# Kernel optimization log

Hardware: AMD Instinct MI355X
Metric: run time of the kernel (lower is better)

Reference implementation:

```python
import jax, jax.numpy as jnp
import numpy as np


def hadamard_matrix(n):
    # Recursive normalized Hadamard matrix of size 2^n (matches the torch code).
    H = np.array([[1.0]])
    for _ in range(n):
        H = np.block([[H, H], [H, -H]]) / np.sqrt(2.0)
    return jnp.asarray(H, dtype=jnp.float32)


def hadamard_conv(x, filt, bias, H):
    # x: (B, Cin, h, w); filt: (F, kh, kw); bias: (F, 1); H: (n, n)
    n = H.shape[0]
    F, kh, kw = filt.shape
    B, C = x.shape[0], x.shape[1]
    # zero-pad filters and data up to (n, n), then 2D Hadamard transform H A H
    kern = jnp.zeros((F, n, n), x.dtype).at[:, :kh, :kw].set(filt)
    kern_t = jnp.matmul(H, jnp.matmul(kern, H))            # (F, n, n)
    data = jnp.zeros((B, C, n, n), x.dtype).at[:, :, : x.shape[2], : x.shape[3]].set(x)
    data_t = jnp.matmul(H, jnp.matmul(data, H))            # (B, C, n, n)
    # Original: expand to (B, C, F, n, n), multiply by kern_t, inverse transform,
    # then sum over C. Since kern_t is independent of C and the transforms are
    # linear, sum over C first -- identical math, no huge intermediate.
    s = data_t.sum(axis=1)                                  # (B, n, n)
    prod = s[:, None, :, :] * kern_t[None, :, :, :]         # (B, F, n, n)
    out = jnp.matmul(H, jnp.matmul(prod, H))                # (B, F, n, n)
    return out + bias[:, 0][None, :, None, None]


def maxpool2(x):
    # 2x2 max pool, stride 2, on (B, C, H, W)
    return jax.lax.reduce_window(x, -jnp.inf, jax.lax.max, (1, 1, 2, 2), (1, 1, 2, 2), 'VALID')


def setup_inputs() -> dict:
    key = jax.random.key(0)
    ks = jax.random.split(key, 9)
    return {
        'x': jax.random.normal(ks[0], (2048, 3, 32, 32), dtype=jnp.float32),
        'filter1': jax.random.normal(ks[1], (32, 3, 3), dtype=jnp.float32),
        'bias1': jax.random.normal(ks[2], (32, 1), dtype=jnp.float32),
        'filter2': jax.random.normal(ks[3], (64, 3, 3), dtype=jnp.float32),
        'bias2': jax.random.normal(ks[4], (64, 1), dtype=jnp.float32),
        'fc1_w': jax.random.normal(ks[5], (512, 4096), dtype=jnp.float32) * 0.02,
        'fc1_b': jax.random.normal(ks[6], (512,), dtype=jnp.float32) * 0.02,
        'fc2_w': jax.random.normal(ks[7], (10, 512), dtype=jnp.float32) * 0.02,
        'fc2_b': jax.random.normal(ks[8], (10,), dtype=jnp.float32) * 0.02,
    }


def reference(x, filter1, bias1, filter2, bias2, fc1_w, fc1_b, fc2_w, fc2_b):
    H1 = hadamard_matrix(5)  # 32x32
    H2 = hadamard_matrix(4)  # 16x16
    out = hadamard_conv(x, filter1, bias1, H1)      # (B, 32, 32, 32)
    out = maxpool2(jax.nn.relu(out))                # (B, 32, 16, 16)
    out = hadamard_conv(out, filter2, bias2, H2)    # (B, 64, 16, 16)
    out = maxpool2(jax.nn.relu(out))                # (B, 64, 8, 8)
    out = out.reshape(-1, 4096)
    out = jax.nn.relu(out @ fc1_w.T + fc1_b)        # (B, 512)
    out = out @ fc2_w.T + fc2_b                     # (B, 10)
    return jax.nn.softmax(out, axis=1)
```

## Files before the change

### kernel.cpp

```cpp
#include <hip/hip_runtime.h>

#define DEVI __device__ __forceinline__

typedef __attribute__((ext_vector_type(8))) short short8x;
typedef __attribute__((ext_vector_type(4))) float float4x;

DEVI float shx(float v, int m) { return __shfl_xor(v, m, 64); }

DEVI unsigned bf16r(float v) {
  unsigned u = __float_as_uint(v);
  return (u + 0x7FFF + ((u >> 16) & 1)) >> 16;
}
DEVI void split2(float a, float b, unsigned& h, unsigned& l) {
  unsigned ra = bf16r(a), rb = bf16r(b);
  float fa = __uint_as_float(ra << 16), fb = __uint_as_float(rb << 16);
  unsigned la = bf16r(a - fa), lb = bf16r(b - fb);
  h = ra | (rb << 16);
  l = la | (lb << 16);
}

DEVI void gload16(const void* g, void* l) {
  __builtin_amdgcn_global_load_lds(
      (const __attribute__((address_space(1))) void*)g,
      (__attribute__((address_space(3))) void*)l, 16, 0, 0);
}

template <int MASK>
DEVI float lanex(float x) {
  if constexpr (MASK == 1)
    return __int_as_float(__builtin_amdgcn_update_dpp(
        0, __float_as_int(x), 0xB1, 0xF, 0xF, true));
  else if constexpr (MASK == 2)
    return __int_as_float(__builtin_amdgcn_update_dpp(
        0, __float_as_int(x), 0x4E, 0xF, 0xF, true));
  else
    return __int_as_float(__builtin_amdgcn_ds_swizzle(
        __float_as_int(x), (MASK << 10) | 0x1F));
}

__global__ __launch_bounds__(256) void k_conv(
    const float* __restrict__ x, const float* __restrict__ filt1,
    const float* __restrict__ bias1, const float* __restrict__ filt2,
    const float* __restrict__ bias2, unsigned short* __restrict__ Ah,
    unsigned short* __restrict__ Al) {
  __shared__ float sP[4 * 320];
  const int b = blockIdx.x;
  const int tid = threadIdx.x;
  const int wv = tid >> 6, t = tid & 63;

  float s0[16];
  {
    const float* xb = x + (size_t)b * 3072 + (t >> 1) * 32 + (t & 1) * 16;
#pragma unroll
    for (int q = 0; q < 4; ++q) {
      float4 a0 = *(const float4*)(xb + 4 * q);
      float4 a1 = *(const float4*)(xb + 1024 + 4 * q);
      float4 a2 = *(const float4*)(xb + 2048 + 4 * q);
      s0[4 * q + 0] = a0.x + a1.x + a2.x;
      s0[4 * q + 1] = a0.y + a1.y + a2.y;
      s0[4 * q + 2] = a0.z + a1.z + a2.z;
      s0[4 * q + 3] = a0.w + a1.w + a2.w;
    }
  }
  float s1[16], s2[16];
#pragma unroll
  for (int k = 0; k < 16; ++k) s1[k] = lanex<2>(s0[k]);
#pragma unroll
  for (int k = 0; k < 16; ++k) s2[k] = lanex<4>(s0[k]);

  float acc[8];
#pragma unroll
  for (int j = 0; j < 8; ++j) acc[j] = 0.0f;

  for (int i = 0; i < 8; ++i) {
    const int f = __builtin_amdgcn_readfirstlane(wv * 8 + i);
    const float* fp = filt1 + f * 9;
    float w[9];
#pragma unroll
    for (int k = 0; k < 9; ++k) w[k] = fp[k] * (1.0f / 32.0f);
    const float bb = bias1[f];
    float u[16];
#pragma unroll
    for (int jj = 0; jj < 16; ++jj) {
      const int j1 = jj ^ 1, j2 = jj ^ 2;
      float v = fmaf(w[0], s0[jj], bb);
      v = fmaf(w[1], s0[j1], v);
      v = fmaf(w[2], s0[j2], v);
      v = fmaf(w[3], s1[jj], v);
      v = fmaf(w[4], s1[j1], v);
      v = fmaf(w[5], s1[j2], v);
      v = fmaf(w[6], s2[jj], v);
      v = fmaf(w[7], s2[j1], v);
      v = fmaf(w[8], s2[j2], v);
      u[jj] = fmaxf(v, 0.0f);
    }
#pragma unroll
    for (int k = 0; k < 16; ++k) u[k] = fmaxf(u[k], lanex<2>(u[k]));
#pragma unroll
    for (int j = 0; j < 8; ++j) acc[j] += fmaxf(u[2 * j], u[2 * j + 1]);
  }

  if (!(t & 2)) {
    const int pb = wv * 320 + (t >> 2) * 20 + (t & 1) * 8;
    *(float4*)&sP[pb] = make_float4(acc[0], acc[1], acc[2], acc[3]);
    *(float4*)&sP[pb + 4] = make_float4(acc[4], acc[5], acc[6], acc[7]);
  }
  __syncthreads();

  const int f2s = t >> 4, rr = t & 15;
  float r0[16];
#pragma unroll
  for (int q = 0; q < 4; ++q) {
    float4 s = make_float4(0.f, 0.f, 0.f, 0.f);
#pragma unroll
    for (int w2 = 0; w2 < 4; ++w2) {
      const float4 v = *(const float4*)&sP[w2 * 320 + rr * 20 + 4 * q];
      s.x += v.x; s.y += v.y; s.z += v.z; s.w += v.w;
    }
    r0[4 * q + 0] = s.x;
    r0[4 * q + 1] = s.y;
    r0[4 * q + 2] = s.z;
    r0[4 * q + 3] = s.w;
  }
  float r1[16], r2[16];
#pragma unroll
  for (int k = 0; k < 16; ++k) r1[k] = lanex<1>(r0[k]);
#pragma unroll
  for (int k = 0; k < 16; ++k) r2[k] = lanex<2>(r0[k]);

#pragma unroll
  for (int it = 0; it < 4; ++it) {
    const int g = wv * 16 + it * 4 + f2s;
    const float* gp = filt2 + g * 9;
    float w[9];
#pragma unroll
    for (int k = 0; k < 9; ++k) w[k] = gp[k] * (1.0f / 16.0f);
    const float bb = bias2[g];
    float u[16];
#pragma unroll
    for (int jj = 0; jj < 16; ++jj) {
      const int j1 = jj ^ 1, j2 = jj ^ 2;
      float v = fmaf(w[0], r0[jj], bb);
      v = fmaf(w[1], r0[j1], v);
      v = fmaf(w[2], r0[j2], v);
      v = fmaf(w[3], r1[jj], v);
      v = fmaf(w[4], r1[j1], v);
      v = fmaf(w[5], r1[j2], v);
      v = fmaf(w[6], r2[jj], v);
      v = fmaf(w[7], r2[j1], v);
      v = fmaf(w[8], r2[j2], v);
      u[jj] = fmaxf(v, 0.0f);
    }
#pragma unroll
    for (int k = 0; k < 16; ++k) u[k] = fmaxf(u[k], lanex<1>(u[k]));
    float p[8];
#pragma unroll
    for (int j = 0; j < 8; ++j) p[j] = fmaxf(u[2 * j], u[2 * j + 1]);
    if (!(t & 1)) {
      unsigned hh[4], ll[4];
#pragma unroll
      for (int j = 0; j < 4; ++j) split2(p[2 * j], p[2 * j + 1], hh[j], ll[j]);
      const size_t off = (size_t)b * 4096 + g * 64 + (rr >> 1) * 8;
      *(uint4*)(Ah + off) = make_uint4(hh[0], hh[1], hh[2], hh[3]);
      *(uint4*)(Al + off) = make_uint4(ll[0], ll[1], ll[2], ll[3]);
    }
  }
}

__global__ __launch_bounds__(256) void k_wsplit(
    const float* __restrict__ W, unsigned short* __restrict__ Wh,
    unsigned short* __restrict__ Wl) {
  const int i = (blockIdx.x * 256 + threadIdx.x) * 4;
  float4 v = *(const float4*)(W + i);
  unsigned h0, l0, h1, l1;
  split2(v.x, v.y, h0, l0);
  split2(v.z, v.w, h1, l1);
  *(uint2*)(Wh + i) = make_uint2(h0, h1);
  *(uint2*)(Wl + i) = make_uint2(l0, l1);
}

__global__ __launch_bounds__(256) void k_fc1(
    const unsigned short* __restrict__ Ah, const unsigned short* __restrict__ Al,
    const unsigned short* __restrict__ Wh, const unsigned short* __restrict__ Wl,
    float* __restrict__ P, int M) {
  __shared__ __align__(16) unsigned char lds[49152];
  const int bid = blockIdx.x;
  const int low3 = bid & 7, rest = bid >> 3;
  const int nt = rest & 7;
  const int c = ((rest >> 3) << 3) | low3;
  const int mt = c >> 2, kidx = c & 3;
  const int m0 = mt * 128, n0 = nt * 64, k0 = kidx * 1024;

  const int tid = threadIdx.x;
  const int wv = tid >> 6, lane = tid & 63;
  const int wm = (wv >> 1) * 64, wn = (wv & 1) * 32;
  const int lm = lane & 15, lq = lane >> 4;
  const int lr = lane >> 3, lc = lane & 7;

  float4x acc[4][2];
#pragma unroll
  for (int i = 0; i < 4; ++i)
#pragma unroll
    for (int j = 0; j < 2; ++j) acc[i][j] = (float4x){0.f, 0.f, 0.f, 0.f};

  for (int kk = 0; kk < 1024; kk += 64) {
    const int kcol = k0 + kk;
#pragma unroll
    for (int it = 0; it < 4; ++it) {
      const int rbase = wv * 32 + it * 8;
      const int r = rbase + lr;
      const size_t go = (size_t)(m0 + r) * 4096 + kcol + (lc ^ (r & 7)) * 8;
      gload16(Ah + go, lds + rbase * 128);
      gload16(Al + go, lds + 16384 + rbase * 128);
    }
#pragma unroll
    for (int it = 0; it < 2; ++it) {
      const int rbase = wv * 16 + it * 8;
      const int r = rbase + lr;
      const size_t go = (size_t)(n0 + r) * 4096 + kcol + (lc ^ (r & 7)) * 8;
      gload16(Wh + go, lds + 32768 + rbase * 128);
      gload16(Wl + go, lds + 40960 + rbase * 128);
    }
    __syncthreads();

    const uint4* l4 = (const uint4*)lds;
#pragma unroll
    for (int ks = 0; ks < 2; ++ks) {
      const int ch = ks * 4 + lq;
      short8x a_h[4], a_l[4], b_h[2], b_l[2];
#pragma unroll
      for (int fm = 0; fm < 4; ++fm) {
        const int r = wm + fm * 16 + lm;
        const int s = r * 8 + (ch ^ (r & 7));
        a_h[fm] = *(const short8x*)&l4[s];
        a_l[fm] = *(const short8x*)&l4[1024 + s];
      }
#pragma unroll
      for (int fn = 0; fn < 2; ++fn) {
        const int r = wn + fn * 16 + lm;
        const int s = r * 8 + (ch ^ (r & 7));
        b_h[fn] = *(const short8x*)&l4[2048 + s];
        b_l[fn] = *(const short8x*)&l4[2560 + s];
      }
#pragma unroll
      for (int fm = 0; fm < 4; ++fm)
#pragma unroll
        for (int fn = 0; fn < 2; ++fn) {
          acc[fm][fn] = __builtin_amdgcn_mfma_f32_16x16x32_bf16(
              a_h[fm], b_h[fn], acc[fm][fn], 0, 0, 0);
          acc[fm][fn] = __builtin_amdgcn_mfma_f32_16x16x32_bf16(
              a_h[fm], b_l[fn], acc[fm][fn], 0, 0, 0);
          acc[fm][fn] = __builtin_amdgcn_mfma_f32_16x16x32_bf16(
              a_l[fm], b_h[fn], acc[fm][fn], 0, 0, 0);
        }
    }
    __syncthreads();
  }

  float* Pp = P + (size_t)kidx * ((size_t)M * 512);
#pragma unroll
  for (int fm = 0; fm < 4; ++fm)
#pragma unroll
    for (int fn = 0; fn < 2; ++fn)
#pragma unroll
      for (int i = 0; i < 4; ++i) {
        const int r = m0 + wm + fm * 16 + lq * 4 + i;
        const int cc = n0 + wn + fn * 16 + lm;
        Pp[(size_t)r * 512 + cc] = acc[fm][fn][i];
      }
}

__global__ __launch_bounds__(256) void k_fc1red4(
    const float* __restrict__ P, const float* __restrict__ bias,
    float* __restrict__ O, int total) {
  const int idx = (blockIdx.x * 256 + threadIdx.x) * 4;
  const float4 p0 = *(const float4*)(P + idx);
  const float4 p1 = *(const float4*)(P + (size_t)total + idx);
  const float4 p2 = *(const float4*)(P + (size_t)2 * total + idx);
  const float4 p3 = *(const float4*)(P + (size_t)3 * total + idx);
  const float4 bv = *(const float4*)(bias + (idx & 511));
  float4 o;
  o.x = fmaxf(p0.x + p1.x + p2.x + p3.x + bv.x, 0.0f);
  o.y = fmaxf(p0.y + p1.y + p2.y + p3.y + bv.y, 0.0f);
  o.z = fmaxf(p0.z + p1.z + p2.z + p3.z + bv.z, 0.0f);
  o.w = fmaxf(p0.w + p1.w + p2.w + p3.w + bv.w, 0.0f);
  *(float4*)(O + idx) = o;
}

__global__ __launch_bounds__(256) void k_fc2(
    const float* __restrict__ X, const float* __restrict__ W,
    const float* __restrict__ bias, float* __restrict__ out) {
  const int wv = threadIdx.x >> 6, t = threadIdx.x & 63;
  const int b = blockIdx.x * 4 + wv;
  const float* xr = X + (size_t)b * 512 + t * 8;
  const float4 x0 = *(const float4*)xr;
  const float4 x1 = *(const float4*)(xr + 4);
  float z[10];
#pragma unroll
  for (int o = 0; o < 10; ++o) {
    const float* wr = W + o * 512 + t * 8;
    const float4 w0 = *(const float4*)wr;
    const float4 w1 = *(const float4*)(wr + 4);
    float s = x0.x * w0.x;
    s = fmaf(x0.y, w0.y, s);
    s = fmaf(x0.z, w0.z, s);
    s = fmaf(x0.w, w0.w, s);
    s = fmaf(x1.x, w1.x, s);
    s = fmaf(x1.y, w1.y, s);
    s = fmaf(x1.z, w1.z, s);
    s = fmaf(x1.w, w1.w, s);
    z[o] = s;
  }
#pragma unroll
  for (int m = 1; m < 64; m <<= 1) {
#pragma unroll
    for (int o = 0; o < 10; ++o) z[o] += shx(z[o], m);
  }
#pragma unroll
  for (int o = 0; o < 10; ++o) z[o] += bias[o];
  float mx = z[0];
#pragma unroll
  for (int o = 1; o < 10; ++o) mx = fmaxf(mx, z[o]);
  float e[10];
  float ssum = 0.0f;
#pragma unroll
  for (int o = 0; o < 10; ++o) {
    e[o] = expf(z[o] - mx);
    ssum += e[o];
  }
  const float inv = 1.0f / ssum;
  if (t == 0) {
    float* dst = out + (size_t)b * 10;
#pragma unroll
    for (int o = 0; o < 10; ++o) dst[o] = e[o] * inv;
  }
}

extern "C" void kernel_launch(void* const* d_in, const int* in_sizes, int n_in,
                              void* d_out, int out_size, void* d_ws,
                              size_t ws_size, hipStream_t stream) {
  const float* x = (const float*)d_in[0];
  const float* f1 = (const float*)d_in[1];
  const float* b1 = (const float*)d_in[2];
  const float* f2 = (const float*)d_in[3];
  const float* b2 = (const float*)d_in[4];
  const float* fc1w = (const float*)d_in[5];
  const float* fc1b = (const float*)d_in[6];
  const float* fc2w = (const float*)d_in[7];
  const float* fc2b = (const float*)d_in[8];
  float* out = (float*)d_out;
  const int B = in_sizes[0] / 3072;

  char* w = (char*)d_ws;
  unsigned short* Ah = (unsigned short*)w;
  unsigned short* Al = (unsigned short*)(w + (size_t)B * 8192);
  unsigned short* Wh = (unsigned short*)(w + (size_t)2 * B * 8192);
  unsigned short* Wl = (unsigned short*)(w + (size_t)2 * B * 8192 + 4194304);
  float* P = (float*)(w + (size_t)2 * B * 8192 + 8388608);
  float* fc1o =
      (float*)(w + (size_t)2 * B * 8192 + 8388608 + (size_t)4 * B * 2048);

  hipLaunchKernelGGL(k_wsplit, dim3(2048), dim3(256), 0, stream, fc1w, Wh, Wl);
  hipLaunchKernelGGL(k_conv, dim3(B), dim3(256), 0, stream, x, f1, b1, f2, b2,
                     Ah, Al);
  hipLaunchKernelGGL(k_fc1, dim3((B / 128) * 32), dim3(256), 0, stream, Ah, Al,
                     Wh, Wl, P, B);
  hipLaunchKernelGGL(k_fc1red4, dim3((B * 512) / 1024), dim3(256), 0, stream,
                     P, fc1b, fc1o, B * 512);
  hipLaunchKernelGGL(k_fc2, dim3(B / 4), dim3(256), 0, stream, fc1o, fc2w,
                     fc2b, out);
}
```

Baseline: 155.3 us.

## Double-buffer fc1 K-loop, fuse fc1 reduction into fc2, streamline conv pooling

The fc1 GEMM now stages 32-wide K slices into two LDS buffers, prefetching the next slice while MFMAs run on the current one. Hi and lo bf16 halves share one swizzled 128-byte row. The separate split-K reduction kernel is removed: fc2 now sums the four partials, adds bias1 and applies ReLU itself, which saves a launch and a global round trip. In the conv kernel, the Hadamard scale moves from the weights to the summed inputs, and ReLU/horizontal max are applied pairwise to cut shuffles and max ops. The trade-off is one extra barrier interval of LDS pressure and slight rounding differences.

```diff
diff --git a/kernel.cpp b/kernel.cpp
--- a/kernel.cpp
+++ b/kernel.cpp
@@ -56,10 +56,10 @@
       float4 a0 = *(const float4*)(xb + 4 * q);
       float4 a1 = *(const float4*)(xb + 1024 + 4 * q);
       float4 a2 = *(const float4*)(xb + 2048 + 4 * q);
-      s0[4 * q + 0] = a0.x + a1.x + a2.x;
-      s0[4 * q + 1] = a0.y + a1.y + a2.y;
-      s0[4 * q + 2] = a0.z + a1.z + a2.z;
-      s0[4 * q + 3] = a0.w + a1.w + a2.w;
+      s0[4 * q + 0] = (a0.x + a1.x + a2.x) * (1.0f / 32.0f);
+      s0[4 * q + 1] = (a0.y + a1.y + a2.y) * (1.0f / 32.0f);
+      s0[4 * q + 2] = (a0.z + a1.z + a2.z) * (1.0f / 32.0f);
+      s0[4 * q + 3] = (a0.w + a1.w + a2.w) * (1.0f / 32.0f);
     }
   }
   float s1[16], s2[16];
@@ -77,27 +77,35 @@
     const float* fp = filt1 + f * 9;
     float w[9];
 #pragma unroll
-    for (int k = 0; k < 9; ++k) w[k] = fp[k] * (1.0f / 32.0f);
+    for (int k = 0; k < 9; ++k) w[k] = fp[k];
     const float bb = bias1[f];
-    float u[16];
-#pragma unroll
-    for (int jj = 0; jj < 16; ++jj) {
-      const int j1 = jj ^ 1, j2 = jj ^ 2;
-      float v = fmaf(w[0], s0[jj], bb);
-      v = fmaf(w[1], s0[j1], v);
-      v = fmaf(w[2], s0[j2], v);
-      v = fmaf(w[3], s1[jj], v);
-      v = fmaf(w[4], s1[j1], v);
-      v = fmaf(w[5], s1[j2], v);
-      v = fmaf(w[6], s2[jj], v);
-      v = fmaf(w[7], s2[j1], v);
-      v = fmaf(w[8], s2[j2], v);
-      u[jj] = fmaxf(v, 0.0f);
-    }
-#pragma unroll
-    for (int k = 0; k < 16; ++k) u[k] = fmaxf(u[k], lanex<2>(u[k]));
-#pragma unroll
-    for (int j = 0; j < 8; ++j) acc[j] += fmaxf(u[2 * j], u[2 * j + 1]);
+    float c[8];
+#pragma unroll
+    for (int p = 0; p < 8; ++p) {
+      const int ja = 2 * p, jb = ja ^ 1;
+      const int ja2 = ja ^ 2, jb2 = jb ^ 2;
+      float va = fmaf(w[0], s0[ja], bb);
+      va = fmaf(w[1], s0[jb], va);
+      va = fmaf(w[2], s0[ja2], va);
+      va = fmaf(w[3], s1[ja], va);
+      va = fmaf(w[4], s1[jb], va);
+      va = fmaf(w[5], s1[ja2], va);
+      va = fmaf(w[6], s2[ja], va);
+      va = fmaf(w[7], s2[jb], va);
+      va = fmaf(w[8], s2[ja2], va);
+      float vb = fmaf(w[0], s0[jb], bb);
+      vb = fmaf(w[1], s0[ja], vb);
+      vb = fmaf(w[2], s0[jb2], vb);
+      vb = fmaf(w[3], s1[jb], vb);
+      vb = fmaf(w[4], s1[ja], vb);
+      vb = fmaf(w[5], s1[jb2], vb);
+      vb = fmaf(w[6], s2[jb], vb);
+      vb = fmaf(w[7], s2[ja], vb);
+      vb = fmaf(w[8], s2[jb2], vb);
+      c[p] = fmaxf(fmaxf(va, vb), 0.0f);
+    }
+#pragma unroll
+    for (int p = 0; p < 8; ++p) acc[p] += fmaxf(c[p], lanex<2>(c[p]));
   }
 
   if (!(t & 2)) {
@@ -117,10 +125,10 @@
       const float4 v = *(const float4*)&sP[w2 * 320 + rr * 20 + 4 * q];
       s.x += v.x; s.y += v.y; s.z += v.z; s.w += v.w;
     }
-    r0[4 * q + 0] = s.x;
-    r0[4 * q + 1] = s.y;
-    r0[4 * q + 2] = s.z;
-    r0[4 * q + 3] = s.w;
+    r0[4 * q + 0] = s.x * (1.0f / 16.0f);
+    r0[4 * q + 1] = s.y * (1.0f / 16.0f);
+    r0[4 * q + 2] = s.z * (1.0f / 16.0f);
+    r0[4 * q + 3] = s.w * (1.0f / 16.0f);
   }
   float r1[16], r2[16];
 #pragma unroll
@@ -134,32 +142,39 @@
     const float* gp = filt2 + g * 9;
     float w[9];
 #pragma unroll
-    for (int k = 0; k < 9; ++k) w[k] = gp[k] * (1.0f / 16.0f);
+    for (int k = 0; k < 9; ++k) w[k] = gp[k];
     const float bb = bias2[g];
-    float u[16];
-#pragma unroll
-    for (int jj = 0; jj < 16; ++jj) {
-      const int j1 = jj ^ 1, j2 = jj ^ 2;
-      float v = fmaf(w[0], r0[jj], bb);
-      v = fmaf(w[1], r0[j1], v);
-      v = fmaf(w[2], r0[j2], v);
-      v = fmaf(w[3], r1[jj], v);
-      v = fmaf(w[4], r1[j1], v);
-      v = fmaf(w[5], r1[j2], v);
-      v = fmaf(w[6], r2[jj], v);
-      v = fmaf(w[7], r2[j1], v);
-      v = fmaf(w[8], r2[j2], v);
-      u[jj] = fmaxf(v, 0.0f);
-    }
-#pragma unroll
-    for (int k = 0; k < 16; ++k) u[k] = fmaxf(u[k], lanex<1>(u[k]));
-    float p[8];
-#pragma unroll
-    for (int j = 0; j < 8; ++j) p[j] = fmaxf(u[2 * j], u[2 * j + 1]);
+    float c[8];
+#pragma unroll
+    for (int p = 0; p < 8; ++p) {
+      const int ja = 2 * p, jb = ja ^ 1;
+      const int ja2 = ja ^ 2, jb2 = jb ^ 2;
+      float va = fmaf(w[0], r0[ja], bb);
+      va = fmaf(w[1], r0[jb], va);
+      va = fmaf(w[2], r0[ja2], va);
+      va = fmaf(w[3], r1[ja], va);
+      va = fmaf(w[4], r1[jb], va);
+      va = fmaf(w[5], r1[ja2], va);
+      va = fmaf(w[6], r2[ja], va);
+      va = fmaf(w[7], r2[jb], va);
+      va = fmaf(w[8], r2[ja2], va);
+      float vb = fmaf(w[0], r0[jb], bb);
+      vb = fmaf(w[1], r0[ja], vb);
+      vb = fmaf(w[2], r0[jb2], vb);
+      vb = fmaf(w[3], r1[jb], vb);
+      vb = fmaf(w[4], r1[ja], vb);
+      vb = fmaf(w[5], r1[jb2], vb);
+      vb = fmaf(w[6], r2[jb], vb);
+      vb = fmaf(w[7], r2[ja], vb);
+      vb = fmaf(w[8], r2[jb2], vb);
+      c[p] = fmaxf(fmaxf(va, vb), 0.0f);
+    }
+#pragma unroll
+    for (int p = 0; p < 8; ++p) c[p] = fmaxf(c[p], lanex<1>(c[p]));
     if (!(t & 1)) {
       unsigned hh[4], ll[4];
 #pragma unroll
-      for (int j = 0; j < 4; ++j) split2(p[2 * j], p[2 * j + 1], hh[j], ll[j]);
+      for (int j = 0; j < 4; ++j) split2(c[2 * j], c[2 * j + 1], hh[j], ll[j]);
       const size_t off = (size_t)b * 4096 + g * 64 + (rr >> 1) * 8;
       *(uint4*)(Ah + off) = make_uint4(hh[0], hh[1], hh[2], hh[3]);
       *(uint4*)(Al + off) = make_uint4(ll[0], ll[1], ll[2], ll[3]);
@@ -195,7 +210,6 @@
   const int wv = tid >> 6, lane = tid & 63;
   const int wm = (wv >> 1) * 64, wn = (wv & 1) * 32;
   const int lm = lane & 15, lq = lane >> 4;
-  const int lr = lane >> 3, lc = lane & 7;
 
   float4x acc[4][2];
 #pragma unroll
@@ -203,57 +217,63 @@
 #pragma unroll
     for (int j = 0; j < 2; ++j) acc[i][j] = (float4x){0.f, 0.f, 0.f, 0.f};
 
-  for (int kk = 0; kk < 1024; kk += 64) {
-    const int kcol = k0 + kk;
+  auto stage = [&](int st, int bb) {
+    const int kcol = k0 + st * 32;
+    const int rj = lane >> 3;
+    const int pj = lane & 7;
 #pragma unroll
     for (int it = 0; it < 4; ++it) {
-      const int rbase = wv * 32 + it * 8;
-      const int r = rbase + lr;
-      const size_t go = (size_t)(m0 + r) * 4096 + kcol + (lc ^ (r & 7)) * 8;
-      gload16(Ah + go, lds + rbase * 128);
-      gload16(Al + go, lds + 16384 + rbase * 128);
+      const int rb = wv * 32 + it * 8;
+      const int r = rb + rj;
+      const int l = pj ^ (r & 7);
+      const unsigned short* src = (l < 4) ? Ah : Al;
+      const size_t go = (size_t)(m0 + r) * 4096 + kcol + (l & 3) * 8;
+      gload16(src + go, lds + bb + rb * 128);
     }
 #pragma unroll
     for (int it = 0; it < 2; ++it) {
-      const int rbase = wv * 16 + it * 8;
-      const int r = rbase + lr;
-      const size_t go = (size_t)(n0 + r) * 4096 + kcol + (lc ^ (r & 7)) * 8;
-      gload16(Wh + go, lds + 32768 + rbase * 128);
-      gload16(Wl + go, lds + 40960 + rbase * 128);
-    }
-    __syncthreads();
-
-    const uint4* l4 = (const uint4*)lds;
-#pragma unroll
-    for (int ks = 0; ks < 2; ++ks) {
-      const int ch = ks * 4 + lq;
-      short8x a_h[4], a_l[4], b_h[2], b_l[2];
-#pragma unroll
-      for (int fm = 0; fm < 4; ++fm) {
-        const int r = wm + fm * 16 + lm;
-        const int s = r * 8 + (ch ^ (r & 7));
-        a_h[fm] = *(const short8x*)&l4[s];
-        a_l[fm] = *(const short8x*)&l4[1024 + s];
+      const int rb = wv * 16 + it * 8;
+      const int r = rb + rj;
+      const int l = pj ^ (r & 7);
+      const unsigned short* src = (l < 4) ? Wh : Wl;
+      const size_t go = (size_t)(n0 + r) * 4096 + kcol + (l & 3) * 8;
+      gload16(src + go, lds + bb + 16384 + rb * 128);
+    }
+  };
+
+  stage(0, 0);
+  __syncthreads();
+
+  for (int st = 0; st < 32; ++st) {
+    const int bb = (st & 1) * 24576;
+    if (st < 31) stage(st + 1, bb ^ 24576);
+
+    short8x a_h[4], a_l[4], b_h[2], b_l[2];
+#pragma unroll
+    for (int fm = 0; fm < 4; ++fm) {
+      const int r = wm + fm * 16 + lm;
+      const unsigned char* base = lds + bb + r * 128;
+      a_h[fm] = *(const short8x*)(base + (lq ^ (r & 7)) * 16);
+      a_l[fm] = *(const short8x*)(base + ((lq ^ 4) ^ (r & 7)) * 16);
+    }
+#pragma unroll
+    for (int fn = 0; fn < 2; ++fn) {
+      const int r = wn + fn * 16 + lm;
+      const unsigned char* base = lds + bb + 16384 + r * 128;
+      b_h[fn] = *(const short8x*)(base + (lq ^ (r & 7)) * 16);
+      b_l[fn] = *(const short8x*)(base + ((lq ^ 4) ^ (r & 7)) * 16);
+    }
+#pragma unroll
+    for (int fm = 0; fm < 4; ++fm)
+#pragma unroll
+      for (int fn = 0; fn < 2; ++fn) {
+        acc[fm][fn] = __builtin_amdgcn_mfma_f32_16x16x32_bf16(
+            a_h[fm], b_h[fn], acc[fm][fn], 0, 0, 0);
+        acc[fm][fn] = __builtin_amdgcn_mfma_f32_16x16x32_bf16(
+            a_h[fm], b_l[fn], acc[fm][fn], 0, 0, 0);
+        acc[fm][fn] = __builtin_amdgcn_mfma_f32_16x16x32_bf16(
+            a_l[fm], b_h[fn], acc[fm][fn], 0, 0, 0);
       }
-#pragma unroll
-      for (int fn = 0; fn < 2; ++fn) {
-        const int r = wn + fn * 16 + lm;
-        const int s = r * 8 + (ch ^ (r & 7));
-        b_h[fn] = *(const short8x*)&l4[2048 + s];
-        b_l[fn] = *(const short8x*)&l4[2560 + s];
-      }
-#pragma unroll
-      for (int fm = 0; fm < 4; ++fm)
-#pragma unroll
-        for (int fn = 0; fn < 2; ++fn) {
-          acc[fm][fn] = __builtin_amdgcn_mfma_f32_16x16x32_bf16(
-              a_h[fm], b_h[fn], acc[fm][fn], 0, 0, 0);
-          acc[fm][fn] = __builtin_amdgcn_mfma_f32_16x16x32_bf16(
-              a_h[fm], b_l[fn], acc[fm][fn], 0, 0, 0);
-          acc[fm][fn] = __builtin_amdgcn_mfma_f32_16x16x32_bf16(
-              a_l[fm], b_h[fn], acc[fm][fn], 0, 0, 0);
-        }
-    }
     __syncthreads();
   }
 
@@ -270,45 +290,48 @@
       }
 }
 
-__global__ __launch_bounds__(256) void k_fc1red4(
-    const float* __restrict__ P, const float* __restrict__ bias,
-    float* __restrict__ O, int total) {
-  const int idx = (blockIdx.x * 256 + threadIdx.x) * 4;
-  const float4 p0 = *(const float4*)(P + idx);
-  const float4 p1 = *(const float4*)(P + (size_t)total + idx);
-  const float4 p2 = *(const float4*)(P + (size_t)2 * total + idx);
-  const float4 p3 = *(const float4*)(P + (size_t)3 * total + idx);
-  const float4 bv = *(const float4*)(bias + (idx & 511));
-  float4 o;
-  o.x = fmaxf(p0.x + p1.x + p2.x + p3.x + bv.x, 0.0f);
-  o.y = fmaxf(p0.y + p1.y + p2.y + p3.y + bv.y, 0.0f);
-  o.z = fmaxf(p0.z + p1.z + p2.z + p3.z + bv.z, 0.0f);
-  o.w = fmaxf(p0.w + p1.w + p2.w + p3.w + bv.w, 0.0f);
-  *(float4*)(O + idx) = o;
-}
-
 __global__ __launch_bounds__(256) void k_fc2(
-    const float* __restrict__ X, const float* __restrict__ W,
-    const float* __restrict__ bias, float* __restrict__ out) {
+    const float* __restrict__ P, const float* __restrict__ bias1,
+    const float* __restrict__ W, const float* __restrict__ bias2,
+    float* __restrict__ out, int M) {
   const int wv = threadIdx.x >> 6, t = threadIdx.x & 63;
   const int b = blockIdx.x * 4 + wv;
-  const float* xr = X + (size_t)b * 512 + t * 8;
-  const float4 x0 = *(const float4*)xr;
-  const float4 x1 = *(const float4*)(xr + 4);
+  const size_t ks = (size_t)M * 512;
+  const float* pr = P + (size_t)b * 512 + t * 8;
+  float4 u0 = *(const float4*)pr;
+  float4 u1 = *(const float4*)(pr + 4);
+#pragma unroll
+  for (int k = 1; k < 4; ++k) {
+    const float4 v0 = *(const float4*)(pr + k * ks);
+    const float4 v1 = *(const float4*)(pr + k * ks + 4);
+    u0.x += v0.x; u0.y += v0.y; u0.z += v0.z; u0.w += v0.w;
+    u1.x += v1.x; u1.y += v1.y; u1.z += v1.z; u1.w += v1.w;
+  }
+  const float4 bb0 = *(const float4*)(bias1 + t * 8);
+  const float4 bb1 = *(const float4*)(bias1 + t * 8 + 4);
+  float a[8];
+  a[0] = fmaxf(u0.x + bb0.x, 0.0f);
+  a[1] = fmaxf(u0.y + bb0.y, 0.0f);
+  a[2] = fmaxf(u0.z + bb0.z, 0.0f);
+  a[3] = fmaxf(u0.w + bb0.w, 0.0f);
+  a[4] = fmaxf(u1.x + bb1.x, 0.0f);
+  a[5] = fmaxf(u1.y + bb1.y, 0.0f);
+  a[6] = fmaxf(u1.z + bb1.z, 0.0f);
+  a[7] = fmaxf(u1.w + bb1.w, 0.0f);
   float z[10];
 #pragma unroll
   for (int o = 0; o < 10; ++o) {
     const float* wr = W + o * 512 + t * 8;
     const float4 w0 = *(const float4*)wr;
     const float4 w1 = *(const float4*)(wr + 4);
-    float s = x0.x * w0.x;
-    s = fmaf(x0.y, w0.y, s);
-    s = fmaf(x0.z, w0.z, s);
-    s = fmaf(x0.w, w0.w, s);
-    s = fmaf(x1.x, w1.x, s);
-    s = fmaf(x1.y, w1.y, s);
-    s = fmaf(x1.z, w1.z, s);
-    s = fmaf(x1.w, w1.w, s);
+    float s = a[0] * w0.x;
+    s = fmaf(a[1], w0.y, s);
+    s = fmaf(a[2], w0.z, s);
+    s = fmaf(a[3], w0.w, s);
+    s = fmaf(a[4], w1.x, s);
+    s = fmaf(a[5], w1.y, s);
+    s = fmaf(a[6], w1.z, s);
+    s = fmaf(a[7], w1.w, s);
     z[o] = s;
   }
 #pragma unroll
@@ -317,7 +340,7 @@
     for (int o = 0; o < 10; ++o) z[o] += shx(z[o], m);
   }
 #pragma unroll
-  for (int o = 0; o < 10; ++o) z[o] += bias[o];
+  for (int o = 0; o < 10; ++o) z[o] += bias2[o];
   float mx = z[0];
 #pragma unroll
   for (int o = 1; o < 10; ++o) mx = fmaxf(mx, z[o]);
@@ -357,16 +380,12 @@
   unsigned short* Wh = (unsigned short*)(w + (size_t)2 * B * 8192);
   unsigned short* Wl = (unsigned short*)(w + (size_t)2 * B * 8192 + 4194304);
   float* P = (float*)(w + (size_t)2 * B * 8192 + 8388608);
-  float* fc1o =
-      (float*)(w + (size_t)2 * B * 8192 + 8388608 + (size_t)4 * B * 2048);
 
   hipLaunchKernelGGL(k_wsplit, dim3(2048), dim3(256), 0, stream, fc1w, Wh, Wl);
   hipLaunchKernelGGL(k_conv, dim3(B), dim3(256), 0, stream, x, f1, b1, f2, b2,
                      Ah, Al);
   hipLaunchKernelGGL(k_fc1, dim3((B / 128) * 32), dim3(256), 0, stream, Ah, Al,
                      Wh, Wl, P, B);
-  hipLaunchKernelGGL(k_fc1red4, dim3((B * 512) / 1024), dim3(256), 0, stream,
-                     P, fc1b, fc1o, B * 512);
-  hipLaunchKernelGGL(k_fc2, dim3(B / 4), dim3(256), 0, stream, fc1o, fc2w,
-                     fc2b, out);
-}
+  hipLaunchKernelGGL(k_fc2, dim3(B / 4), dim3(256), 0, stream, P, fc1b, fc2w,
+                     fc2b, out, B);
+}
```

Measured after the change: 154.8 us. No clear change (-0.3%).
